# Optimization experiments

Measured on AMD Instinct MI355X. Metric: run time of the kernel, lower is better.

The kernel has to match this reference:

```python
import jax, jax.numpy as jnp
import numpy as np

BS, SEQ, VOCAB, EMS, NHID, ML = 32, 512, 5000, 256, 512, 16
TEMP = 0.9
GAMMA = 0.0  # self.gamma is a fixed zero Variable in the original


def setup_inputs() -> dict:
    key = jax.random.key(0)
    ks = jax.random.split(key, 10)
    nm = SEQ // ML
    inputs = jax.random.randint(ks[0], (BS, SEQ), 0, VOCAB, dtype=jnp.int32)
    measure_steps = jax.random.randint(ks[1], (ML, BS, nm), 0, VOCAB, dtype=jnp.int32)
    measure_weights = jax.random.normal(ks[2], (BS, nm, nm), dtype=jnp.float32)
    h0 = jnp.zeros((BS, NHID), jnp.float32)
    c0 = jnp.zeros((BS, NHID), jnp.float32)
    initrange = 0.1
    emb = jax.random.uniform(ks[3], (VOCAB, EMS), minval=-initrange, maxval=initrange)
    k = 1.0 / np.sqrt(NHID).astype(np.float32)
    W_ih = jax.random.uniform(ks[4], (4 * NHID, EMS), minval=-k, maxval=k)
    W_hh = jax.random.uniform(ks[5], (4 * NHID, NHID), minval=-k, maxval=k)
    b_ih = jax.random.uniform(ks[6], (4 * NHID,), minval=-k, maxval=k)
    b_hh = jax.random.uniform(ks[7], (4 * NHID,), minval=-k, maxval=k)
    W_dec = jax.random.uniform(ks[8], (VOCAB, NHID), minval=-initrange, maxval=initrange)
    b_dec = jnp.zeros((VOCAB,), jnp.float32)
    return dict(inputs=inputs, h0=h0, c0=c0, measure_weights=measure_weights,
                measure_steps=measure_steps, emb=emb, W_ih=W_ih, W_hh=W_hh,
                b_ih=b_ih, b_hh=b_hh, W_dec=W_dec, b_dec=b_dec, measure_length=ML)


def _forward(h0, c0, mw, emb, W_ih, W_hh, b_ih, b_hh, W_dec, b_dec,
             inputs, msteps, measure_length):
    bs, seq = inputs.shape
    nm = seq // measure_length
    # attention over previous measures: softmax over j < m (causal-masked)
    mask = (jnp.arange(nm)[None, :] < jnp.arange(nm)[:, None]).astype(mw.dtype)  # [m, j]
    logits = jnp.where(mask[None] > 0, mw / TEMP, -1e9)
    sm = jax.nn.softmax(logits, axis=-1) * mask[None]  # [bs, m, j]
    prev_embs = emb[msteps]  # [ML, bs, nm, E]
    # lookback embedding for (measure m, step s): sum_j sm[b,m,j] * emb[steps[s,b,j]]
    lb = jnp.einsum('bmj,sbje->msbe', sm, prev_embs)  # [nm, ML, bs, E]
    lb_seq = lb.reshape(seq, bs, -1)  # time-major: t = m*ML + s
    # per-step bmm decode against embedding table: [bs, seq, V]
    lookback = jnp.einsum('tbe,ve->btv', lb_seq, emb)
    # original zeros lookback for timesteps with int(i/num_measures)==0, i.e. i < nm
    tmask = (jnp.arange(seq) >= nm)[None, :, None]
    lookback = jnp.where(tmask, lookback, jnp.zeros((), lookback.dtype))

    x = emb[inputs]  # [bs, seq, E] (single channel -> concat is identity)

    def cell(carry, xt):
        h, c = carry
        g = xt @ W_ih.T + b_ih + h @ W_hh.T + b_hh
        i, f, gg, o = jnp.split(g, 4, axis=-1)
        c2 = jax.nn.sigmoid(f) * c + jax.nn.sigmoid(i) * jnp.tanh(gg)
        h2 = jax.nn.sigmoid(o) * jnp.tanh(c2)
        return (h2, c2), h2

    (hT, cT), hs = jax.lax.scan(cell, (h0, c0), jnp.swapaxes(x, 0, 1))
    out = jnp.swapaxes(hs, 0, 1)  # [bs, seq, nhid]
    decoded = out @ W_dec.T + b_dec  # [bs, seq, V]
    dec = (1.0 - GAMMA) * decoded + GAMMA * lookback
    return dec, hT, cT


def reference(inputs, h0, c0, measure_weights, measure_steps, emb,
              W_ih, W_hh, b_ih, b_hh, W_dec, b_dec, measure_length):
    return _forward(h0, c0, measure_weights, emb, W_ih, W_hh, b_ih, b_hh,
                    W_dec, b_dec, inputs, measure_steps, measure_length)
```

## Files before the change

kernel.cpp:

```cpp
#include <hip/hip_runtime.h>
#include <cstdint>
#include <cstddef>

#define BS     32
#define SEQ    512
#define VOCAB  5000
#define EMS    256
#define NHID   512
#define GH     2048
#define NWG    32
#define SLICE  16
#define VPAD   5120
#define NTILE  ((BS*SEQ/128) * (VPAD/128))

#define WS_BIAS  0
#define WS_WIH   (WS_BIAS + GH*4)
#define WS_WHH   (WS_WIH + GH*EMS*2)
#define WS_WDH   (WS_WHH + GH*NHID*2)
#define WS_WDL   (WS_WDH + VPAD*NHID*2)
#define WS_X     (WS_WDL + VPAD*NHID*2)
#define WS_HHI   (WS_X + SEQ*BS*EMS*2)
#define WS_HLO   (WS_HHI + BS*SEQ*NHID*2)
#define WS_TAG   (WS_HLO + BS*SEQ*NHID*2)
#define WS_END   (WS_TAG + 2*8192*8)

typedef float f32x4 __attribute__((ext_vector_type(4)));
typedef __bf16 bf16x8 __attribute__((ext_vector_type(8)));

static __device__ __forceinline__ uint16_t f2bf(float x) {
  uint32_t u = __builtin_bit_cast(uint32_t, x);
  u += 0x7FFFu + ((u >> 16) & 1u);
  return (uint16_t)(u >> 16);
}
static __device__ __forceinline__ float bf2f(uint16_t b) {
  return __builtin_bit_cast(float, (uint32_t)b << 16);
}
static __device__ __forceinline__ float sigf(float x) { return 1.0f / (1.0f + __expf(-x)); }
static __device__ __forceinline__ float tanhf_fast(float x) {
  return 1.0f - 2.0f / (__expf(2.0f * x) + 1.0f);
}
static __device__ __forceinline__ f32x4 mfma16(uint4 a, uint4 b, f32x4 c) {
  return __builtin_amdgcn_mfma_f32_16x16x32_bf16(
      __builtin_bit_cast(bf16x8, a), __builtin_bit_cast(bf16x8, b), c, 0, 0, 0);
}
static __device__ __forceinline__ void glds16(const void* g, void* l) {
  __builtin_amdgcn_global_load_lds((__attribute__((address_space(1))) void*)g,
                                   (__attribute__((address_space(3))) void*)l,
                                   16, 0, 0);
}

__global__ __launch_bounds__(256) void prep_kernel(
    const int* __restrict__ inputs, const float* __restrict__ h0,
    const float* __restrict__ emb, const float* __restrict__ Wih,
    const float* __restrict__ Whh, const float* __restrict__ bih,
    const float* __restrict__ bhh, const float* __restrict__ Wd,
    char* __restrict__ ws) {
  int gid = blockIdx.x * 256 + threadIdx.x;
  int gsz = gridDim.x * 256;
  uint16_t* wX  = (uint16_t*)(ws + WS_X);
  uint16_t* wIH = (uint16_t*)(ws + WS_WIH);
  uint16_t* wHH = (uint16_t*)(ws + WS_WHH);
  uint16_t* wDH = (uint16_t*)(ws + WS_WDH);
  uint16_t* wDL = (uint16_t*)(ws + WS_WDL);
  float*    bias = (float*)(ws + WS_BIAS);
  unsigned long long* Tg = (unsigned long long*)(ws + WS_TAG);
  for (int i = gid; i < SEQ*BS*EMS; i += gsz) {
    int e = i & (EMS-1), b = (i >> 8) & (BS-1), t = i >> 13;
    wX[i] = f2bf(emb[(size_t)inputs[b*SEQ + t] * EMS + e]);
  }
  for (int i = gid; i < GH*EMS; i += gsz)  wIH[i] = f2bf(Wih[i]);
  for (int i = gid; i < GH*NHID; i += gsz) wHH[i] = f2bf(Whh[i]);
  for (int i = gid; i < VPAD*NHID; i += gsz) {
    int row = i >> 9;
    uint16_t hi = 0, lo = 0;
    if (row < VOCAB) {
      float x = Wd[i];
      hi = f2bf(x);
      lo = f2bf(x - bf2f(hi));
    }
    wDH[i] = hi; wDL[i] = lo;
  }
  for (int i = gid; i < GH; i += gsz) bias[i] = bih[i] + bhh[i];
  for (int u = gid; u < 8192; u += gsz) {
    int b = u >> 8, p = u & 255;
    uint32_t pay = (uint32_t)f2bf(h0[b*NHID + 2*p]) |
                   ((uint32_t)f2bf(h0[b*NHID + 2*p + 1]) << 16);
    Tg[u] = (unsigned long long)pay;
    Tg[8192 + u] = 0xFFFFFFFF00000000ull;
  }
}

template <int KSTEPS, int NPASS>
__global__ __launch_bounds__(256) void gemm_kernel(
    const uint16_t* __restrict__ A0, const uint16_t* __restrict__ B0,
    const float* __restrict__ bias, float* __restrict__ out,
    int Nvalid, int ldout) {
  constexpr int K = KSTEPS * 32;
  constexpr int TOT = KSTEPS * NPASS;
  __shared__ __align__(16) char lds[4][8192];
  const int tid = threadIdx.x;
  const int lane = tid & 63, w = tid >> 6;
  const int m0 = blockIdx.y * 128, n0 = blockIdx.x * 128;
  const int wbase = (tid & ~63);

  auto stage = [&](int buf, int s) {
    const int kk = s % KSTEPS;
    char* dA = &lds[buf*2][0];
    char* dB = &lds[buf*2+1][0];
#pragma unroll
    for (int c = 0; c < 2; ++c) {
      int idx = c*256 + tid;
      int row = idx >> 2, col = (idx & 3) * 8;
      glds16(A0 + (size_t)(m0 + row) * K + kk*32 + col, dA + (c*256 + wbase)*16);
      glds16(B0 + (size_t)(n0 + row) * K + kk*32 + col, dB + (c*256 + wbase)*16);
    }
  };

  const f32x4 zero = {0.f, 0.f, 0.f, 0.f};
  f32x4 acc[4][4];
#pragma unroll
  for (int i = 0; i < 4; ++i)
#pragma unroll
    for (int j = 0; j < 4; ++j) acc[i][j] = zero;

  const int mq = (w >> 1) * 64, nq = (w & 1) * 64;
  stage(0, 0);
  for (int s = 0; s < TOT; ++s) {
    __syncthreads();
    if (s + 1 < TOT) stage((s + 1) & 1, s + 1);
    const char* cA = &lds[(s & 1)*2][0];
    const char* cB = &lds[(s & 1)*2+1][0];
    uint4 a[4], b[4];
#pragma unroll
    for (int i = 0; i < 4; ++i) {
      a[i] = *(const uint4*)(cA + (mq + i*16 + (lane & 15))*64 + (lane >> 4)*16);
      b[i] = *(const uint4*)(cB + (nq + i*16 + (lane & 15))*64 + (lane >> 4)*16);
    }
#pragma unroll
    for (int i = 0; i < 4; ++i)
#pragma unroll
      for (int j = 0; j < 4; ++j) acc[i][j] = mfma16(a[i], b[j], acc[i][j]);
  }
#pragma unroll
  for (int j = 0; j < 4; ++j) {
    int V = n0 + nq + j*16 + (lane & 15);
    if (V >= Nvalid) continue;
    float bv = bias[V];
#pragma unroll
    for (int i = 0; i < 4; ++i) {
      int Rb = m0 + mq + i*16 + (lane >> 4)*4;
#pragma unroll
      for (int r = 0; r < 4; ++r)
        out[(size_t)(Rb + r) * ldout + V] = acc[i][j][r] + bv;
    }
  }
}

__global__ __launch_bounds__(256, 1) void scan_kernel(
    const float* __restrict__ Gin, char* __restrict__ ws,
    const float* __restrict__ c0, float* __restrict__ outT) {
  __shared__ __align__(16) char sW[64*1024];
  __shared__ __align__(16) char sH[32*1024];
  __shared__ float sG[4*BS*SLICE];
  const uint16_t* wHH = (const uint16_t*)(ws + WS_WHH);
  unsigned long long* Tg = (unsigned long long*)(ws + WS_TAG);
  uint16_t* Hhi  = (uint16_t*)(ws + WS_HHI);
  uint16_t* Hlo  = (uint16_t*)(ws + WS_HLO);
  const int tid = threadIdx.x, wg = blockIdx.x;
  const int lane = tid & 63, w = tid >> 6;
  const int mw = w >> 1, nw = w & 1;

  for (int c = tid; c < 4096; c += 256) {
    int row = c >> 6;
    int kb = (c & 63) * 16;
    int G = row >> 4, dl = row & 15;
    uint4 v = *(const uint4*)(wHH + (size_t)(G*NHID + wg*SLICE + dl) * NHID + kb/2);
    *(uint4*)(sW + row*1024 + (kb ^ ((row & 7) << 4))) = v;
  }
  const int bq = tid >> 3, dq = (tid & 7) * 2;
  float c_0 = c0[bq*NHID + wg*SLICE + dq];
  float c_1 = c0[bq*NHID + wg*SLICE + dq + 1];
  const int arow = mw*16 + (lane & 15);
  const int brow0 = (2*nw)*16 + (lane & 15);
  const int brow1 = brow0 + 16;
  const int kb0 = (lane >> 4) * 16;
  const int pidx = bq*256 + wg*8 + (tid & 7);

  float ga0[4], ga1[4], gb0[4], gb1[4];
  {
    const float* grow = Gin + wg*SLICE + (lane & 15);
#pragma unroll
    for (int r = 0; r < 4; ++r) {
      int b = mw*16 + (lane >> 4)*4 + r;
      ga0[r] = grow[(size_t)b*GH + (2*nw+0)*NHID];
      ga1[r] = grow[(size_t)b*GH + (2*nw+1)*NHID];
    }
  }
  __syncthreads();

  for (int t = 0; t < SEQ; ++t) {
    if (t + 1 < SEQ) {
      const float* grow = Gin + (size_t)(t+1)*(BS*GH) + wg*SLICE + (lane & 15);
#pragma unroll
      for (int r = 0; r < 4; ++r) {
        int b = mw*16 + (lane >> 4)*4 + r;
        gb0[r] = grow[(size_t)b*GH + (2*nw+0)*NHID];
        gb1[r] = grow[(size_t)b*GH + (2*nw+1)*NHID];
      }
    }

    {
      const char* tb = (const char*)(Tg + (size_t)(t & 1) * 8192) + tid * 16;
      const uint32_t tg = (uint32_t)t;
      uint4 q0, q1, q2, q3, q4, q5, q6, q7, q8, q9, q10, q11, q12, q13, q14, q15;
      uint32_t tries = 0;
      for (;;) {
#define PQ(QJ, OFF) asm volatile("global_load_dwordx4 %0, %1, off sc0 sc1" \
                                 : "=v"(QJ) : "v"(tb + (OFF)));
        PQ(q0, 0)      PQ(q1, 4096)   PQ(q2, 8192)   PQ(q3, 12288)
        PQ(q4, 16384)  PQ(q5, 20480)  PQ(q6, 24576)  PQ(q7, 28672)
        PQ(q8, 32768)  PQ(q9, 36864)  PQ(q10, 40960) PQ(q11, 45056)
        PQ(q12, 49152) PQ(q13, 53248) PQ(q14, 57344) PQ(q15, 61440)
#undef PQ
        asm volatile("s_waitcnt vmcnt(0)" ::: "memory");
        __builtin_amdgcn_sched_barrier(0);
        uint32_t bad =
            (q0.y^tg)|(q0.w^tg)|(q1.y^tg)|(q1.w^tg)|(q2.y^tg)|(q2.w^tg)|(q3.y^tg)|(q3.w^tg)|
            (q4.y^tg)|(q4.w^tg)|(q5.y^tg)|(q5.w^tg)|(q6.y^tg)|(q6.w^tg)|(q7.y^tg)|(q7.w^tg)|
            (q8.y^tg)|(q8.w^tg)|(q9.y^tg)|(q9.w^tg)|(q10.y^tg)|(q10.w^tg)|(q11.y^tg)|(q11.w^tg)|
            (q12.y^tg)|(q12.w^tg)|(q13.y^tg)|(q13.w^tg)|(q14.y^tg)|(q14.w^tg)|(q15.y^tg)|(q15.w^tg);
        if (bad == 0) break;
        if (++tries > (1u << 16)) break;
      }
      const int colb = (tid & 127) * 8;
      const int rh = tid >> 7;
#define STW(J, QJ) { int b = 2*(J) + rh; uint2 wv; wv.x = QJ.x; wv.y = QJ.z; \
      *(uint2*)(sH + b*1024 + (colb ^ ((b & 7) << 4))) = wv; }
      STW(0, q0)   STW(1, q1)   STW(2, q2)   STW(3, q3)
      STW(4, q4)   STW(5, q5)   STW(6, q6)   STW(7, q7)
      STW(8, q8)   STW(9, q9)   STW(10, q10) STW(11, q11)
      STW(12, q12) STW(13, q13) STW(14, q14) STW(15, q15)
#undef STW
    }
    __syncthreads();

    f32x4 acc0, acc1;
#pragma unroll
    for (int r = 0; r < 4; ++r) { acc0[r] = ga0[r]; acc1[r] = ga1[r]; }
#pragma unroll
    for (int kt = 0; kt < 16; ++kt) {
      int kb = kt*64 + kb0;
      uint4 av = *(const uint4*)(sH + arow*1024 + (kb ^ ((arow & 7) << 4)));
      uint4 b0 = *(const uint4*)(sW + brow0*1024 + (kb ^ ((brow0 & 7) << 4)));
      uint4 b1 = *(const uint4*)(sW + brow1*1024 + (kb ^ ((brow1 & 7) << 4)));
      acc0 = mfma16(av, b0, acc0);
      acc1 = mfma16(av, b1, acc1);
    }
#pragma unroll
    for (int r = 0; r < 4; ++r) {
      int b = mw*16 + (lane >> 4)*4 + r;
      sG[((2*nw+0)*BS + b)*SLICE + (lane & 15)] = acc0[r];
      sG[((2*nw+1)*BS + b)*SLICE + (lane & 15)] = acc1[r];
    }
#pragma unroll
    for (int r = 0; r < 4; ++r) { ga0[r] = gb0[r]; ga1[r] = gb1[r]; }
    __syncthreads();

    float gi0 = sG[(0*BS + bq)*SLICE + dq], gi1 = sG[(0*BS + bq)*SLICE + dq + 1];
    float gf0 = sG[(1*BS + bq)*SLICE + dq], gf1 = sG[(1*BS + bq)*SLICE + dq + 1];
    float gg0 = sG[(2*BS + bq)*SLICE + dq], gg1 = sG[(2*BS + bq)*SLICE + dq + 1];
    float go0 = sG[(3*BS + bq)*SLICE + dq], go1 = sG[(3*BS + bq)*SLICE + dq + 1];
    c_0 = sigf(gf0)*c_0 + sigf(gi0)*tanhf_fast(gg0);
    c_1 = sigf(gf1)*c_1 + sigf(gi1)*tanhf_fast(gg1);
    float h_0 = sigf(go0)*tanhf_fast(c_0);
    float h_1 = sigf(go1)*tanhf_fast(c_1);

    uint16_t hh0 = f2bf(h_0), hh1 = f2bf(h_1);
    uint32_t hp = (uint32_t)hh0 | ((uint32_t)hh1 << 16);
    __hip_atomic_store(Tg + (size_t)((t + 1) & 1) * 8192 + pidx,
                       ((unsigned long long)(uint32_t)(t + 1) << 32) | (unsigned long long)hp,
                       __ATOMIC_RELAXED, __HIP_MEMORY_SCOPE_AGENT);
    size_t hoff = ((size_t)bq*SEQ + t)*NHID + wg*SLICE + dq;
    *(uint32_t*)(Hhi + hoff) = hp;
    uint32_t lp = (uint32_t)f2bf(h_0 - bf2f(hh0)) | ((uint32_t)f2bf(h_1 - bf2f(hh1)) << 16);
    *(uint32_t*)(Hlo + hoff) = lp;
    if (t == SEQ-1) {
      outT[bq*NHID + wg*SLICE + dq]     = h_0;
      outT[bq*NHID + wg*SLICE + dq + 1] = h_1;
      outT[BS*NHID + bq*NHID + wg*SLICE + dq]     = c_0;
      outT[BS*NHID + bq*NHID + wg*SLICE + dq + 1] = c_1;
    }
  }
}

__global__ __launch_bounds__(256) void decode_kernel(
    const char* __restrict__ ws, const float* __restrict__ bdec,
    float* __restrict__ out) {
  __shared__ __align__(16) char lds[2][32768];
  const uint16_t* Hhi = (const uint16_t*)(ws + WS_HHI);
  const uint16_t* Hlo = (const uint16_t*)(ws + WS_HLO);
  const uint16_t* WDH = (const uint16_t*)(ws + WS_WDH);
  const uint16_t* WDL = (const uint16_t*)(ws + WS_WDL);
  const int tid = threadIdx.x;
  const int lane = tid & 63, w = tid >> 6;
  const int wbase = (tid & ~63);
  const int mq = (w >> 1) * 64, nq = (w & 1) * 64;
  const int bid = (int)blockIdx.x;
  const int swz = (bid & 7) * (NTILE / 8) + (bid >> 3);
  const int mt = swz / 40, nt = swz % 40;
  const int m0 = mt * 128, n0 = nt * 128;

  auto stage = [&](int buf, int kk) {
    char* base = &lds[buf][0];
#pragma unroll
    for (int c2 = 0; c2 < 2; ++c2) {
      int idx = c2*256 + tid;
      int row = idx >> 2, col = (idx & 3) * 8;
      int ldst = (c2*256 + wbase) * 16;
      glds16(Hhi + (size_t)(m0 + row) * NHID + kk*32 + col, base + ldst);
      glds16(Hlo + (size_t)(m0 + row) * NHID + kk*32 + col, base + 8192 + ldst);
      glds16(WDH + (size_t)(n0 + row) * NHID + kk*32 + col, base + 16384 + ldst);
      glds16(WDL + (size_t)(n0 + row) * NHID + kk*32 + col, base + 24576 + ldst);
    }
  };

  const f32x4 zero = {0.f, 0.f, 0.f, 0.f};
  f32x4 acc[4][4];
#pragma unroll
  for (int i = 0; i < 4; ++i)
#pragma unroll
    for (int j = 0; j < 4; ++j) acc[i][j] = zero;

  stage(0, 0);
  for (int s = 0; s < 16; ++s) {
    __syncthreads();
    if (s + 1 < 16) stage((s + 1) & 1, s + 1);
    const char* cb = &lds[s & 1][0];
    uint4 ahi[4], alo[4], bhi[4], blo[4];
#pragma unroll
    for (int i = 0; i < 4; ++i) {
      int aoff = (mq + i*16 + (lane & 15))*64 + (lane >> 4)*16;
      int boff = (nq + i*16 + (lane & 15))*64 + (lane >> 4)*16;
      ahi[i] = *(const uint4*)(cb + aoff);
      alo[i] = *(const uint4*)(cb + 8192 + aoff);
      bhi[i] = *(const uint4*)(cb + 16384 + boff);
      blo[i] = *(const uint4*)(cb + 24576 + boff);
    }
#pragma unroll
    for (int i = 0; i < 4; ++i)
#pragma unroll
      for (int j = 0; j < 4; ++j) {
        acc[i][j] = mfma16(ahi[i], bhi[j], acc[i][j]);
        acc[i][j] = mfma16(ahi[i], blo[j], acc[i][j]);
        acc[i][j] = mfma16(alo[i], bhi[j], acc[i][j]);
      }
  }
#pragma unroll
  for (int j = 0; j < 4; ++j) {
    int V = n0 + nq + j*16 + (lane & 15);
    if (V >= VOCAB) continue;
    float bv = bdec[V];
#pragma unroll
    for (int i = 0; i < 4; ++i) {
      int Rb = m0 + mq + i*16 + (lane >> 4)*4;
#pragma unroll
      for (int r = 0; r < 4; ++r)
        out[(size_t)(Rb + r) * VOCAB + V] = acc[i][j][r] + bv;
    }
  }
}

extern "C" void kernel_launch(void* const* d_in, const int* in_sizes, int n_in,
                              void* d_out, int out_size, void* d_ws, size_t ws_size,
                              hipStream_t stream) {
  (void)in_sizes; (void)n_in; (void)out_size; (void)ws_size;
  const int*   inputs = (const int*)  d_in[0];
  const float* h0     = (const float*)d_in[1];
  const float* c0     = (const float*)d_in[2];
  const float* emb    = (const float*)d_in[5];
  const float* Wih    = (const float*)d_in[6];
  const float* Whh    = (const float*)d_in[7];
  const float* bih    = (const float*)d_in[8];
  const float* bhh    = (const float*)d_in[9];
  const float* Wdec   = (const float*)d_in[10];
  const float* bdec   = (const float*)d_in[11];
  char* ws   = (char*)d_ws;
  float* out = (float*)d_out;
  float* Gin  = out;
  float* outT = out + (size_t)BS*SEQ*VOCAB;

  prep_kernel<<<512, 256, 0, stream>>>(inputs, h0, emb, Wih, Whh, bih, bhh, Wdec, ws);
  gemm_kernel<8,1><<<dim3(GH/128, (BS*SEQ)/128), 256, 0, stream>>>(
      (const uint16_t*)(ws + WS_X), (const uint16_t*)(ws + WS_WIH),
      (const float*)(ws + WS_BIAS), Gin, GH, GH);
  scan_kernel<<<NWG, 256, 0, stream>>>(Gin, ws, c0, outT);
  decode_kernel<<<NTILE, 256, 0, stream>>>(ws, bdec, out);
}
```

Measured before the change: 2.050 ms.

## Re-lay h exchange buffer dim-major and re-poll only stale chunks

Changes the layout of the tagged cross-workgroup hidden-state exchange buffer from batch-major to hidden-pair-major, so each workgroup's published slice is contiguous and the LDS scatter pattern changes. The spin-wait loop now issues one initial load round, then reloads only the chunks whose tags are stale, with a wave-wide any() exit test. This is meant to cut redundant global traffic and latency in the per-timestep grid synchronisation of the LSTM recurrence. The LDS stores become 32-bit instead of 64-bit, which may add bank conflicts, and the retry limit is raised.

```diff
diff --git a/kernel.cpp b/kernel.cpp
--- a/kernel.cpp
+++ b/kernel.cpp
@@ -82,9 +82,9 @@
   }
   for (int i = gid; i < GH; i += gsz) bias[i] = bih[i] + bhh[i];
   for (int u = gid; u < 8192; u += gsz) {
-    int b = u >> 8, p = u & 255;
-    uint32_t pay = (uint32_t)f2bf(h0[b*NHID + 2*p]) |
-                   ((uint32_t)f2bf(h0[b*NHID + 2*p + 1]) << 16);
+    int dpair = u >> 5, b = u & 31;
+    uint32_t pay = (uint32_t)f2bf(h0[b*NHID + 2*dpair]) |
+                   ((uint32_t)f2bf(h0[b*NHID + 2*dpair + 1]) << 16);
     Tg[u] = (unsigned long long)pay;
     Tg[8192 + u] = 0xFFFFFFFF00000000ull;
   }
@@ -184,7 +184,7 @@
   const int brow0 = (2*nw)*16 + (lane & 15);
   const int brow1 = brow0 + 16;
   const int kb0 = (lane >> 4) * 16;
-  const int pidx = bq*256 + wg*8 + (tid & 7);
+  const int pidx = (wg*8 + (tid & 7))*32 + bq;
 
   float ga0[4], ga1[4], gb0[4], gb1[4];
   {
@@ -213,33 +213,49 @@
       const char* tb = (const char*)(Tg + (size_t)(t & 1) * 8192) + tid * 16;
       const uint32_t tg = (uint32_t)t;
       uint4 q0, q1, q2, q3, q4, q5, q6, q7, q8, q9, q10, q11, q12, q13, q14, q15;
+#define PQ(QJ, KT) asm volatile("global_load_dwordx4 %0, %1, off sc0 sc1" \
+                                : "=v"(QJ) : "v"(tb + (KT)*4096));
+      PQ(q0, 0)   PQ(q1, 1)   PQ(q2, 2)   PQ(q3, 3)
+      PQ(q4, 4)   PQ(q5, 5)   PQ(q6, 6)   PQ(q7, 7)
+      PQ(q8, 8)   PQ(q9, 9)   PQ(q10, 10) PQ(q11, 11)
+      PQ(q12, 12) PQ(q13, 13) PQ(q14, 14) PQ(q15, 15)
+      asm volatile("s_waitcnt vmcnt(0)" ::: "memory");
+      __builtin_amdgcn_sched_barrier(0);
+      uint32_t m;
       uint32_t tries = 0;
       for (;;) {
-#define PQ(QJ, OFF) asm volatile("global_load_dwordx4 %0, %1, off sc0 sc1" \
-                                 : "=v"(QJ) : "v"(tb + (OFF)));
-        PQ(q0, 0)      PQ(q1, 4096)   PQ(q2, 8192)   PQ(q3, 12288)
-        PQ(q4, 16384)  PQ(q5, 20480)  PQ(q6, 24576)  PQ(q7, 28672)
-        PQ(q8, 32768)  PQ(q9, 36864)  PQ(q10, 40960) PQ(q11, 45056)
-        PQ(q12, 49152) PQ(q13, 53248) PQ(q14, 57344) PQ(q15, 61440)
-#undef PQ
+        m = 0;
+#define CHK(QJ, KT) m |= ((((QJ).y ^ tg) | ((QJ).w ^ tg)) != 0u ? 1u : 0u) << (KT);
+        CHK(q0, 0)   CHK(q1, 1)   CHK(q2, 2)   CHK(q3, 3)
+        CHK(q4, 4)   CHK(q5, 5)   CHK(q6, 6)   CHK(q7, 7)
+        CHK(q8, 8)   CHK(q9, 9)   CHK(q10, 10) CHK(q11, 11)
+        CHK(q12, 12) CHK(q13, 13) CHK(q14, 14) CHK(q15, 15)
+#undef CHK
+        if (!__any((int)(m != 0u))) break;
+        if (++tries > (1u << 18)) break;
+#define RQ(QJ, KT) if (m & (1u << (KT))) PQ(QJ, KT)
+        RQ(q0, 0)   RQ(q1, 1)   RQ(q2, 2)   RQ(q3, 3)
+        RQ(q4, 4)   RQ(q5, 5)   RQ(q6, 6)   RQ(q7, 7)
+        RQ(q8, 8)   RQ(q9, 9)   RQ(q10, 10) RQ(q11, 11)
+        RQ(q12, 12) RQ(q13, 13) RQ(q14, 14) RQ(q15, 15)
+#undef RQ
         asm volatile("s_waitcnt vmcnt(0)" ::: "memory");
         __builtin_amdgcn_sched_barrier(0);
-        uint32_t bad =
-            (q0.y^tg)|(q0.w^tg)|(q1.y^tg)|(q1.w^tg)|(q2.y^tg)|(q2.w^tg)|(q3.y^tg)|(q3.w^tg)|
-            (q4.y^tg)|(q4.w^tg)|(q5.y^tg)|(q5.w^tg)|(q6.y^tg)|(q6.w^tg)|(q7.y^tg)|(q7.w^tg)|
-            (q8.y^tg)|(q8.w^tg)|(q9.y^tg)|(q9.w^tg)|(q10.y^tg)|(q10.w^tg)|(q11.y^tg)|(q11.w^tg)|
-            (q12.y^tg)|(q12.w^tg)|(q13.y^tg)|(q13.w^tg)|(q14.y^tg)|(q14.w^tg)|(q15.y^tg)|(q15.w^tg);
-        if (bad == 0) break;
-        if (++tries > (1u << 16)) break;
       }
-      const int colb = (tid & 127) * 8;
-      const int rh = tid >> 7;
-#define STW(J, QJ) { int b = 2*(J) + rh; uint2 wv; wv.x = QJ.x; wv.y = QJ.z; \
-      *(uint2*)(sH + b*1024 + (colb ^ ((b & 7) << 4))) = wv; }
-      STW(0, q0)   STW(1, q1)   STW(2, q2)   STW(3, q3)
-      STW(4, q4)   STW(5, q5)   STW(6, q6)   STW(7, q7)
-      STW(8, q8)   STW(9, q9)   STW(10, q10) STW(11, q11)
-      STW(12, q12) STW(13, q13) STW(14, q14) STW(15, q15)
+#undef PQ
+      const int b0 = 2 * (tid & 15);
+      const int cbase = (tid >> 4) * 4;
+      char* r0 = sH + b0*1024;
+      char* r1 = sH + (b0+1)*1024;
+      const int sw0 = (b0 & 7) << 4;
+      const int sw1 = ((b0+1) & 7) << 4;
+#define STW(QJ, KT) { int cb = (KT)*64 + cbase; \
+      *(uint32_t*)(r0 + (cb ^ sw0)) = (QJ).x; \
+      *(uint32_t*)(r1 + (cb ^ sw1)) = (QJ).z; }
+      STW(q0, 0)   STW(q1, 1)   STW(q2, 2)   STW(q3, 3)
+      STW(q4, 4)   STW(q5, 5)   STW(q6, 6)   STW(q7, 7)
+      STW(q8, 8)   STW(q9, 9)   STW(q10, 10) STW(q11, 11)
+      STW(q12, 12) STW(q13, 13) STW(q14, 14) STW(q15, 15)
 #undef STW
     }
     __syncthreads();
@@ -251,10 +267,10 @@
     for (int kt = 0; kt < 16; ++kt) {
       int kb = kt*64 + kb0;
       uint4 av = *(const uint4*)(sH + arow*1024 + (kb ^ ((arow & 7) << 4)));
-      uint4 b0 = *(const uint4*)(sW + brow0*1024 + (kb ^ ((brow0 & 7) << 4)));
-      uint4 b1 = *(const uint4*)(sW + brow1*1024 + (kb ^ ((brow1 & 7) << 4)));
-      acc0 = mfma16(av, b0, acc0);
-      acc1 = mfma16(av, b1, acc1);
+      uint4 b0v = *(const uint4*)(sW + brow0*1024 + (kb ^ ((brow0 & 7) << 4)));
+      uint4 b1v = *(const uint4*)(sW + brow1*1024 + (kb ^ ((brow1 & 7) << 4)));
+      acc0 = mfma16(av, b0v, acc0);
+      acc1 = mfma16(av, b1v, acc1);
     }
 #pragma unroll
     for (int r = 0; r < 4; ++r) {
```

Measured after the change: 2.339 ms. +14.1%, slower.

## Restructure LSTM scan into 64 single-wave workgroups split by batch half

Applied to the files above, without the earlier changes.

The recurrent scan now runs 64 single-wavefront workgroups, each owning a 16-hidden slice for one half of the batch, instead of 32 four-wave workgroups. Each wave computes all four gates with MFMA and applies the cell update straight from registers, which removes the LDS gate exchange and both __syncthreads per step. The tag buffer layout is regrouped per batch half so each wave polls only the 32 KB it needs, with a wave-wide any() check. The cost is twice as many workgroups polling and writing flags, plus shuffles to pack the bf16 pairs; each wave also loads the full 64 KB weight slice.

```diff
diff --git a/kernel.cpp b/kernel.cpp
--- a/kernel.cpp
+++ b/kernel.cpp
@@ -8,7 +8,6 @@
 #define EMS    256
 #define NHID   512
 #define GH     2048
-#define NWG    32
 #define SLICE  16
 #define VPAD   5120
 #define NTILE  ((BS*SEQ/128) * (VPAD/128))
@@ -82,9 +81,11 @@
   }
   for (int i = gid; i < GH; i += gsz) bias[i] = bih[i] + bhh[i];
   for (int u = gid; u < 8192; u += gsz) {
-    int b = u >> 8, p = u & 255;
-    uint32_t pay = (uint32_t)f2bf(h0[b*NHID + 2*p]) |
-                   ((uint32_t)f2bf(h0[b*NHID + 2*p + 1]) << 16);
+    int mm = u >> 12, n = u & 4095;
+    int D = n >> 4, bp = n & 15;
+    int b = mm*16 + bp;
+    uint32_t pay = (uint32_t)f2bf(h0[b*NHID + 2*D]) |
+                   ((uint32_t)f2bf(h0[b*NHID + 2*D + 1]) << 16);
     Tg[u] = (unsigned long long)pay;
     Tg[8192 + u] = 0xFFFFFFFF00000000ull;
   }
@@ -156,139 +157,140 @@
   }
 }
 
-__global__ __launch_bounds__(256, 1) void scan_kernel(
+__global__ __launch_bounds__(64, 1) void scan_kernel(
     const float* __restrict__ Gin, char* __restrict__ ws,
     const float* __restrict__ c0, float* __restrict__ outT) {
   __shared__ __align__(16) char sW[64*1024];
-  __shared__ __align__(16) char sH[32*1024];
-  __shared__ float sG[4*BS*SLICE];
+  __shared__ __align__(16) char sH[16*1024];
   const uint16_t* wHH = (const uint16_t*)(ws + WS_WHH);
   unsigned long long* Tg = (unsigned long long*)(ws + WS_TAG);
-  uint16_t* Hhi  = (uint16_t*)(ws + WS_HHI);
-  uint16_t* Hlo  = (uint16_t*)(ws + WS_HLO);
-  const int tid = threadIdx.x, wg = blockIdx.x;
-  const int lane = tid & 63, w = tid >> 6;
-  const int mw = w >> 1, nw = w & 1;
-
-  for (int c = tid; c < 4096; c += 256) {
+  uint16_t* Hhi = (uint16_t*)(ws + WS_HHI);
+  uint16_t* Hlo = (uint16_t*)(ws + WS_HLO);
+  const int lane = threadIdx.x;
+  const int s = (int)blockIdx.x & 31, m = (int)blockIdx.x >> 5;
+  for (int c = lane; c < 4096; c += 64) {
     int row = c >> 6;
     int kb = (c & 63) * 16;
-    int G = row >> 4, dl = row & 15;
-    uint4 v = *(const uint4*)(wHH + (size_t)(G*NHID + wg*SLICE + dl) * NHID + kb/2);
+    int g = row >> 4, dl = row & 15;
+    uint4 v = *(const uint4*)(wHH + (size_t)(g*NHID + s*SLICE + dl) * NHID + kb/2);
     *(uint4*)(sW + row*1024 + (kb ^ ((row & 7) << 4))) = v;
   }
-  const int bq = tid >> 3, dq = (tid & 7) * 2;
-  float c_0 = c0[bq*NHID + wg*SLICE + dq];
-  float c_1 = c0[bq*NHID + wg*SLICE + dq + 1];
-  const int arow = mw*16 + (lane & 15);
-  const int brow0 = (2*nw)*16 + (lane & 15);
-  const int brow1 = brow0 + 16;
-  const int kb0 = (lane >> 4) * 16;
-  const int pidx = bq*256 + wg*8 + (tid & 7);
-
-  float ga0[4], ga1[4], gb0[4], gb1[4];
-  {
-    const float* grow = Gin + wg*SLICE + (lane & 15);
-#pragma unroll
-    for (int r = 0; r < 4; ++r) {
-      int b = mw*16 + (lane >> 4)*4 + r;
-      ga0[r] = grow[(size_t)b*GH + (2*nw+0)*NHID];
-      ga1[r] = grow[(size_t)b*GH + (2*nw+1)*NHID];
-    }
-  }
-  __syncthreads();
+  const int il = lane & 15, kq = lane >> 4;
+  const int d = s*16 + il;
+  const int bbase = m*16 + kq*4;
+  float cst[4];
+#pragma unroll
+  for (int r = 0; r < 4; ++r) cst[r] = c0[(bbase + r)*NHID + d];
+  float ga[16], gb[16];
+#pragma unroll
+  for (int g = 0; g < 4; ++g)
+#pragma unroll
+    for (int r = 0; r < 4; ++r)
+      ga[g*4+r] = Gin[(size_t)(bbase + r)*GH + g*NHID + d];
+  const int b0r = (2*lane) & 15, b1r = b0r + 1;
+  char* sr0 = sH + b0r*1024;
+  char* sr1 = sH + b1r*1024;
+  const int sw0 = (b0r & 7) << 4, sw1 = (b1r & 7) << 4;
 
   for (int t = 0; t < SEQ; ++t) {
     if (t + 1 < SEQ) {
-      const float* grow = Gin + (size_t)(t+1)*(BS*GH) + wg*SLICE + (lane & 15);
-#pragma unroll
-      for (int r = 0; r < 4; ++r) {
-        int b = mw*16 + (lane >> 4)*4 + r;
-        gb0[r] = grow[(size_t)b*GH + (2*nw+0)*NHID];
-        gb1[r] = grow[(size_t)b*GH + (2*nw+1)*NHID];
-      }
-    }
-
+      const float* gr = Gin + (size_t)(t+1)*(BS*GH) + d;
+#pragma unroll
+      for (int g = 0; g < 4; ++g)
+#pragma unroll
+        for (int r = 0; r < 4; ++r)
+          gb[g*4+r] = gr[(size_t)(bbase + r)*GH + g*NHID];
+    }
     {
-      const char* tb = (const char*)(Tg + (size_t)(t & 1) * 8192) + tid * 16;
+      const char* tb = (const char*)(Tg + (size_t)(t & 1)*8192 + (size_t)m*4096) + lane*16;
       const uint32_t tg = (uint32_t)t;
-      uint4 q0, q1, q2, q3, q4, q5, q6, q7, q8, q9, q10, q11, q12, q13, q14, q15;
+      uint4 q0,q1,q2,q3,q4,q5,q6,q7,q8,q9,q10,q11,q12,q13,q14,q15;
+      uint4 q16,q17,q18,q19,q20,q21,q22,q23,q24,q25,q26,q27,q28,q29,q30,q31;
       uint32_t tries = 0;
       for (;;) {
-#define PQ(QJ, OFF) asm volatile("global_load_dwordx4 %0, %1, off sc0 sc1" \
-                                 : "=v"(QJ) : "v"(tb + (OFF)));
-        PQ(q0, 0)      PQ(q1, 4096)   PQ(q2, 8192)   PQ(q3, 12288)
-        PQ(q4, 16384)  PQ(q5, 20480)  PQ(q6, 24576)  PQ(q7, 28672)
-        PQ(q8, 32768)  PQ(q9, 36864)  PQ(q10, 40960) PQ(q11, 45056)
-        PQ(q12, 49152) PQ(q13, 53248) PQ(q14, 57344) PQ(q15, 61440)
+#define PQ(QJ, J) asm volatile("global_load_dwordx4 %0, %1, off sc0 sc1" \
+                               : "=v"(QJ) : "v"(tb + (J)*1024));
+        PQ(q0,0) PQ(q1,1) PQ(q2,2) PQ(q3,3) PQ(q4,4) PQ(q5,5) PQ(q6,6) PQ(q7,7)
+        PQ(q8,8) PQ(q9,9) PQ(q10,10) PQ(q11,11) PQ(q12,12) PQ(q13,13) PQ(q14,14) PQ(q15,15)
+        PQ(q16,16) PQ(q17,17) PQ(q18,18) PQ(q19,19) PQ(q20,20) PQ(q21,21) PQ(q22,22) PQ(q23,23)
+        PQ(q24,24) PQ(q25,25) PQ(q26,26) PQ(q27,27) PQ(q28,28) PQ(q29,29) PQ(q30,30) PQ(q31,31)
 #undef PQ
         asm volatile("s_waitcnt vmcnt(0)" ::: "memory");
         __builtin_amdgcn_sched_barrier(0);
         uint32_t bad =
-            (q0.y^tg)|(q0.w^tg)|(q1.y^tg)|(q1.w^tg)|(q2.y^tg)|(q2.w^tg)|(q3.y^tg)|(q3.w^tg)|
-            (q4.y^tg)|(q4.w^tg)|(q5.y^tg)|(q5.w^tg)|(q6.y^tg)|(q6.w^tg)|(q7.y^tg)|(q7.w^tg)|
-            (q8.y^tg)|(q8.w^tg)|(q9.y^tg)|(q9.w^tg)|(q10.y^tg)|(q10.w^tg)|(q11.y^tg)|(q11.w^tg)|
-            (q12.y^tg)|(q12.w^tg)|(q13.y^tg)|(q13.w^tg)|(q14.y^tg)|(q14.w^tg)|(q15.y^tg)|(q15.w^tg);
-        if (bad == 0) break;
-        if (++tries > (1u << 16)) break;
+          (q0.y^tg)|(q0.w^tg)|(q1.y^tg)|(q1.w^tg)|(q2.y^tg)|(q2.w^tg)|(q3.y^tg)|(q3.w^tg)|
+          (q4.y^tg)|(q4.w^tg)|(q5.y^tg)|(q5.w^tg)|(q6.y^tg)|(q6.w^tg)|(q7.y^tg)|(q7.w^tg)|
+          (q8.y^tg)|(q8.w^tg)|(q9.y^tg)|(q9.w^tg)|(q10.y^tg)|(q10.w^tg)|(q11.y^tg)|(q11.w^tg)|
+          (q12.y^tg)|(q12.w^tg)|(q13.y^tg)|(q13.w^tg)|(q14.y^tg)|(q14.w^tg)|(q15.y^tg)|(q15.w^tg)|
+          (q16.y^tg)|(q16.w^tg)|(q17.y^tg)|(q17.w^tg)|(q18.y^tg)|(q18.w^tg)|(q19.y^tg)|(q19.w^tg)|
+          (q20.y^tg)|(q20.w^tg)|(q21.y^tg)|(q21.w^tg)|(q22.y^tg)|(q22.w^tg)|(q23.y^tg)|(q23.w^tg)|
+          (q24.y^tg)|(q24.w^tg)|(q25.y^tg)|(q25.w^tg)|(q26.y^tg)|(q26.w^tg)|(q27.y^tg)|(q27.w^tg)|
+          (q28.y^tg)|(q28.w^tg)|(q29.y^tg)|(q29.w^tg)|(q30.y^tg)|(q30.w^tg)|(q31.y^tg)|(q31.w^tg);
+        if (!__any((int)(bad != 0u))) break;
+        if (++tries > (1u << 14)) break;
       }
-      const int colb = (tid & 127) * 8;
-      const int rh = tid >> 7;
-#define STW(J, QJ) { int b = 2*(J) + rh; uint2 wv; wv.x = QJ.x; wv.y = QJ.z; \
-      *(uint2*)(sH + b*1024 + (colb ^ ((b & 7) << 4))) = wv; }
-      STW(0, q0)   STW(1, q1)   STW(2, q2)   STW(3, q3)
-      STW(4, q4)   STW(5, q5)   STW(6, q6)   STW(7, q7)
-      STW(8, q8)   STW(9, q9)   STW(10, q10) STW(11, q11)
-      STW(12, q12) STW(13, q13) STW(14, q14) STW(15, q15)
+#define STW(QJ, J) { int cb = ((J)*8 + (lane >> 3)) * 4; \
+      *(uint32_t*)(sr0 + (cb ^ sw0)) = (QJ).x; \
+      *(uint32_t*)(sr1 + (cb ^ sw1)) = (QJ).z; }
+      STW(q0,0) STW(q1,1) STW(q2,2) STW(q3,3) STW(q4,4) STW(q5,5) STW(q6,6) STW(q7,7)
+      STW(q8,8) STW(q9,9) STW(q10,10) STW(q11,11) STW(q12,12) STW(q13,13) STW(q14,14) STW(q15,15)
+      STW(q16,16) STW(q17,17) STW(q18,18) STW(q19,19) STW(q20,20) STW(q21,21) STW(q22,22) STW(q23,23)
+      STW(q24,24) STW(q25,25) STW(q26,26) STW(q27,27) STW(q28,28) STW(q29,29) STW(q30,30) STW(q31,31)
 #undef STW
     }
-    __syncthreads();
-
-    f32x4 acc0, acc1;
-#pragma unroll
-    for (int r = 0; r < 4; ++r) { acc0[r] = ga0[r]; acc1[r] = ga1[r]; }
+    f32x4 a0, a1, a2, a3;
+#pragma unroll
+    for (int r = 0; r < 4; ++r) {
+      a0[r] = ga[0*4+r]; a1[r] = ga[1*4+r]; a2[r] = ga[2*4+r]; a3[r] = ga[3*4+r];
+    }
 #pragma unroll
     for (int kt = 0; kt < 16; ++kt) {
-      int kb = kt*64 + kb0;
-      uint4 av = *(const uint4*)(sH + arow*1024 + (kb ^ ((arow & 7) << 4)));
-      uint4 b0 = *(const uint4*)(sW + brow0*1024 + (kb ^ ((brow0 & 7) << 4)));
-      uint4 b1 = *(const uint4*)(sW + brow1*1024 + (kb ^ ((brow1 & 7) << 4)));
-      acc0 = mfma16(av, b0, acc0);
-      acc1 = mfma16(av, b1, acc1);
-    }
+      int kb = (kt*64 + kq*16) ^ ((il & 7) << 4);
+      uint4 av  = *(const uint4*)(sH + il*1024 + kb);
+      uint4 bv0 = *(const uint4*)(sW + (0*16 + il)*1024 + kb);
+      uint4 bv1 = *(const uint4*)(sW + (1*16 + il)*1024 + kb);
+      uint4 bv2 = *(const uint4*)(sW + (2*16 + il)*1024 + kb);
+      uint4 bv3 = *(const uint4*)(sW + (3*16 + il)*1024 + kb);
+      a0 = mfma16(av, bv0, a0);
+      a1 = mfma16(av, bv1, a1);
+      a2 = mfma16(av, bv2, a2);
+      a3 = mfma16(av, bv3, a3);
+    }
+#pragma unroll
+    for (int k = 0; k < 16; ++k) ga[k] = gb[k];
+
+    float hr[4];
 #pragma unroll
     for (int r = 0; r < 4; ++r) {
-      int b = mw*16 + (lane >> 4)*4 + r;
-      sG[((2*nw+0)*BS + b)*SLICE + (lane & 15)] = acc0[r];
-      sG[((2*nw+1)*BS + b)*SLICE + (lane & 15)] = acc1[r];
-    }
-#pragma unroll
-    for (int r = 0; r < 4; ++r) { ga0[r] = gb0[r]; ga1[r] = gb1[r]; }
-    __syncthreads();
-
-    float gi0 = sG[(0*BS + bq)*SLICE + dq], gi1 = sG[(0*BS + bq)*SLICE + dq + 1];
-    float gf0 = sG[(1*BS + bq)*SLICE + dq], gf1 = sG[(1*BS + bq)*SLICE + dq + 1];
-    float gg0 = sG[(2*BS + bq)*SLICE + dq], gg1 = sG[(2*BS + bq)*SLICE + dq + 1];
-    float go0 = sG[(3*BS + bq)*SLICE + dq], go1 = sG[(3*BS + bq)*SLICE + dq + 1];
-    c_0 = sigf(gf0)*c_0 + sigf(gi0)*tanhf_fast(gg0);
-    c_1 = sigf(gf1)*c_1 + sigf(gi1)*tanhf_fast(gg1);
-    float h_0 = sigf(go0)*tanhf_fast(c_0);
-    float h_1 = sigf(go1)*tanhf_fast(c_1);
-
-    uint16_t hh0 = f2bf(h_0), hh1 = f2bf(h_1);
-    uint32_t hp = (uint32_t)hh0 | ((uint32_t)hh1 << 16);
-    __hip_atomic_store(Tg + (size_t)((t + 1) & 1) * 8192 + pidx,
-                       ((unsigned long long)(uint32_t)(t + 1) << 32) | (unsigned long long)hp,
-                       __ATOMIC_RELAXED, __HIP_MEMORY_SCOPE_AGENT);
-    size_t hoff = ((size_t)bq*SEQ + t)*NHID + wg*SLICE + dq;
-    *(uint32_t*)(Hhi + hoff) = hp;
-    uint32_t lp = (uint32_t)f2bf(h_0 - bf2f(hh0)) | ((uint32_t)f2bf(h_1 - bf2f(hh1)) << 16);
-    *(uint32_t*)(Hlo + hoff) = lp;
+      float cv = sigf(a1[r])*cst[r] + sigf(a0[r])*tanhf_fast(a2[r]);
+      hr[r] = sigf(a3[r])*tanhf_fast(cv);
+      cst[r] = cv;
+    }
+#pragma unroll
+    for (int r = 0; r < 4; ++r) {
+      uint16_t hh = f2bf(hr[r]);
+      float lo = hr[r] - bf2f(hh);
+      float hn = __shfl_xor(hr[r], 1);
+      float ln = __shfl_xor(lo, 1);
+      if ((lane & 1) == 0) {
+        uint32_t pay = (uint32_t)hh | ((uint32_t)f2bf(hn) << 16);
+        uint32_t lop = (uint32_t)f2bf(lo) | ((uint32_t)f2bf(ln) << 16);
+        int bp = kq*4 + r;
+        int n = (s*8 + (il >> 1))*16 + bp;
+        __hip_atomic_store(Tg + (size_t)((t + 1) & 1)*8192 + (size_t)m*4096 + n,
+            ((unsigned long long)(uint32_t)(t + 1) << 32) | (unsigned long long)pay,
+            __ATOMIC_RELAXED, __HIP_MEMORY_SCOPE_AGENT);
+        size_t hoff = ((size_t)(m*16 + bp)*SEQ + t)*NHID + d;
+        *(uint32_t*)(Hhi + hoff) = pay;
+        *(uint32_t*)(Hlo + hoff) = lop;
+      }
+    }
     if (t == SEQ-1) {
-      outT[bq*NHID + wg*SLICE + dq]     = h_0;
-      outT[bq*NHID + wg*SLICE + dq + 1] = h_1;
-      outT[BS*NHID + bq*NHID + wg*SLICE + dq]     = c_0;
-      outT[BS*NHID + bq*NHID + wg*SLICE + dq + 1] = c_1;
+#pragma unroll
+      for (int r = 0; r < 4; ++r) {
+        outT[(bbase + r)*NHID + d] = hr[r];
+        outT[BS*NHID + (bbase + r)*NHID + d] = cst[r];
+      }
     }
   }
 }
@@ -393,6 +395,6 @@
   gemm_kernel<8,1><<<dim3(GH/128, (BS*SEQ)/128), 256, 0, stream>>>(
       (const uint16_t*)(ws + WS_X), (const uint16_t*)(ws + WS_WIH),
       (const float*)(ws + WS_BIAS), Gin, GH, GH);
-  scan_kernel<<<NWG, 256, 0, stream>>>(Gin, ws, c0, outT);
+  scan_kernel<<<64, 64, 0, stream>>>(Gin, ws, c0, outT);
   decode_kernel<<<NTILE, 256, 0, stream>>>(ws, bdec, out);
 }
```

Result: slower. 2.873 ms (+40.1%).

## Replace tagged h-payload polling with per-workgroup step flags and plain h buffer

Applied to the files above, without the earlier changes.

The recurrent scan no longer publishes each hidden-state pair as a 64-bit word carrying a step tag. Each workgroup now writes bf16 h into a double-buffered plain buffer, runs a block barrier, and then bumps its own step flag. Consumers spin on the 32 flags (one lane per workgroup) and then do a single non-retrying load of half the previous data volume. This cuts the polled bytes per step, but each step now needs two serial global round trips (flag poll, then data load) plus an extra barrier. There is also no release fence between the h stores and the relaxed flag store, so visibility ordering is not guaranteed.

```diff
diff --git a/kernel.cpp b/kernel.cpp
--- a/kernel.cpp
+++ b/kernel.cpp
@@ -13,7 +13,8 @@
 #define VPAD   5120
 #define NTILE  ((BS*SEQ/128) * (VPAD/128))
 
-#define WS_BIAS  0
+#define WS_FLAGS 0
+#define WS_BIAS  2048
 #define WS_WIH   (WS_BIAS + GH*4)
 #define WS_WHH   (WS_WIH + GH*EMS*2)
 #define WS_WDH   (WS_WHH + GH*NHID*2)
@@ -21,8 +22,8 @@
 #define WS_X     (WS_WDL + VPAD*NHID*2)
 #define WS_HHI   (WS_X + SEQ*BS*EMS*2)
 #define WS_HLO   (WS_HHI + BS*SEQ*NHID*2)
-#define WS_TAG   (WS_HLO + BS*SEQ*NHID*2)
-#define WS_END   (WS_TAG + 2*8192*8)
+#define WS_HBUF  (WS_HLO + BS*SEQ*NHID*2)
+#define WS_END   (WS_HBUF + 2*BS*NHID*2)
 
 typedef float f32x4 __attribute__((ext_vector_type(4)));
 typedef __bf16 bf16x8 __attribute__((ext_vector_type(8)));
@@ -47,6 +48,9 @@
   __builtin_amdgcn_global_load_lds((__attribute__((address_space(1))) void*)g,
                                    (__attribute__((address_space(3))) void*)l,
                                    16, 0, 0);
+}
+static __device__ __forceinline__ void coh_store_u32(uint32_t* p, uint32_t v) {
+  __hip_atomic_store(p, v, __ATOMIC_RELAXED, __HIP_MEMORY_SCOPE_AGENT);
 }
 
 __global__ __launch_bounds__(256) void prep_kernel(
@@ -63,7 +67,8 @@
   uint16_t* wDH = (uint16_t*)(ws + WS_WDH);
   uint16_t* wDL = (uint16_t*)(ws + WS_WDL);
   float*    bias = (float*)(ws + WS_BIAS);
-  unsigned long long* Tg = (unsigned long long*)(ws + WS_TAG);
+  uint16_t* hb  = (uint16_t*)(ws + WS_HBUF);
+  if (gid < 512) ((uint32_t*)(ws + WS_FLAGS))[gid] = 0u;
   for (int i = gid; i < SEQ*BS*EMS; i += gsz) {
     int e = i & (EMS-1), b = (i >> 8) & (BS-1), t = i >> 13;
     wX[i] = f2bf(emb[(size_t)inputs[b*SEQ + t] * EMS + e]);
@@ -81,13 +86,7 @@
     wDH[i] = hi; wDL[i] = lo;
   }
   for (int i = gid; i < GH; i += gsz) bias[i] = bih[i] + bhh[i];
-  for (int u = gid; u < 8192; u += gsz) {
-    int b = u >> 8, p = u & 255;
-    uint32_t pay = (uint32_t)f2bf(h0[b*NHID + 2*p]) |
-                   ((uint32_t)f2bf(h0[b*NHID + 2*p + 1]) << 16);
-    Tg[u] = (unsigned long long)pay;
-    Tg[8192 + u] = 0xFFFFFFFF00000000ull;
-  }
+  for (int i = gid; i < BS*NHID; i += gsz) hb[i] = f2bf(h0[i]);
 }
 
 template <int KSTEPS, int NPASS>
@@ -163,9 +162,10 @@
   __shared__ __align__(16) char sH[32*1024];
   __shared__ float sG[4*BS*SLICE];
   const uint16_t* wHH = (const uint16_t*)(ws + WS_WHH);
-  unsigned long long* Tg = (unsigned long long*)(ws + WS_TAG);
+  uint16_t* hbuf = (uint16_t*)(ws + WS_HBUF);
   uint16_t* Hhi  = (uint16_t*)(ws + WS_HHI);
   uint16_t* Hlo  = (uint16_t*)(ws + WS_HLO);
+  uint32_t* flags = (uint32_t*)(ws + WS_FLAGS);
   const int tid = threadIdx.x, wg = blockIdx.x;
   const int lane = tid & 63, w = tid >> 6;
   const int mw = w >> 1, nw = w & 1;
@@ -184,7 +184,6 @@
   const int brow0 = (2*nw)*16 + (lane & 15);
   const int brow1 = brow0 + 16;
   const int kb0 = (lane >> 4) * 16;
-  const int pidx = bq*256 + wg*8 + (tid & 7);
 
   float ga0[4], ga1[4], gb0[4], gb1[4];
   {
@@ -199,6 +198,17 @@
   __syncthreads();
 
   for (int t = 0; t < SEQ; ++t) {
+    if (t > 0) {
+      const uint32_t tgt = (uint32_t)t;
+      const uint32_t* fp = flags + (lane & 31) * 16;
+      uint32_t ptries = 0;
+      for (;;) {
+        uint32_t v = __hip_atomic_load(fp, __ATOMIC_RELAXED, __HIP_MEMORY_SCOPE_AGENT);
+        if (__all((int)(v >= tgt))) break;
+        if (++ptries > (1u << 20)) break;
+      }
+    }
+
     if (t + 1 < SEQ) {
       const float* grow = Gin + (size_t)(t+1)*(BS*GH) + wg*SLICE + (lane & 15);
 #pragma unroll
@@ -210,36 +220,24 @@
     }
 
     {
-      const char* tb = (const char*)(Tg + (size_t)(t & 1) * 8192) + tid * 16;
-      const uint32_t tg = (uint32_t)t;
-      uint4 q0, q1, q2, q3, q4, q5, q6, q7, q8, q9, q10, q11, q12, q13, q14, q15;
-      uint32_t tries = 0;
-      for (;;) {
-#define PQ(QJ, OFF) asm volatile("global_load_dwordx4 %0, %1, off sc0 sc1" \
-                                 : "=v"(QJ) : "v"(tb + (OFF)));
-        PQ(q0, 0)      PQ(q1, 4096)   PQ(q2, 8192)   PQ(q3, 12288)
-        PQ(q4, 16384)  PQ(q5, 20480)  PQ(q6, 24576)  PQ(q7, 28672)
-        PQ(q8, 32768)  PQ(q9, 36864)  PQ(q10, 40960) PQ(q11, 45056)
-        PQ(q12, 49152) PQ(q13, 53248) PQ(q14, 57344) PQ(q15, 61440)
-#undef PQ
-        asm volatile("s_waitcnt vmcnt(0)" ::: "memory");
-        __builtin_amdgcn_sched_barrier(0);
-        uint32_t bad =
-            (q0.y^tg)|(q0.w^tg)|(q1.y^tg)|(q1.w^tg)|(q2.y^tg)|(q2.w^tg)|(q3.y^tg)|(q3.w^tg)|
-            (q4.y^tg)|(q4.w^tg)|(q5.y^tg)|(q5.w^tg)|(q6.y^tg)|(q6.w^tg)|(q7.y^tg)|(q7.w^tg)|
-            (q8.y^tg)|(q8.w^tg)|(q9.y^tg)|(q9.w^tg)|(q10.y^tg)|(q10.w^tg)|(q11.y^tg)|(q11.w^tg)|
-            (q12.y^tg)|(q12.w^tg)|(q13.y^tg)|(q13.w^tg)|(q14.y^tg)|(q14.w^tg)|(q15.y^tg)|(q15.w^tg);
-        if (bad == 0) break;
-        if (++tries > (1u << 16)) break;
-      }
-      const int colb = (tid & 127) * 8;
-      const int rh = tid >> 7;
-#define STW(J, QJ) { int b = 2*(J) + rh; uint2 wv; wv.x = QJ.x; wv.y = QJ.z; \
-      *(uint2*)(sH + b*1024 + (colb ^ ((b & 7) << 4))) = wv; }
-      STW(0, q0)   STW(1, q1)   STW(2, q2)   STW(3, q3)
-      STW(4, q4)   STW(5, q5)   STW(6, q6)   STW(7, q7)
-      STW(8, q8)   STW(9, q9)   STW(10, q10) STW(11, q11)
-      STW(12, q12) STW(13, q13) STW(14, q14) STW(15, q15)
+      const char* hsrc = (const char*)(hbuf + (t & 1) * (BS*NHID));
+      const char* pb = hsrc + tid * 16;
+      uint4 v0, v1, v2, v3, v4, v5, v6, v7;
+      asm volatile("global_load_dwordx4 %0, %1, off sc0 sc1" : "=v"(v0) : "v"(pb));
+      asm volatile("global_load_dwordx4 %0, %1, off sc0 sc1" : "=v"(v1) : "v"(pb + 4096));
+      asm volatile("global_load_dwordx4 %0, %1, off sc0 sc1" : "=v"(v2) : "v"(pb + 8192));
+      asm volatile("global_load_dwordx4 %0, %1, off sc0 sc1" : "=v"(v3) : "v"(pb + 12288));
+      asm volatile("global_load_dwordx4 %0, %1, off sc0 sc1" : "=v"(v4) : "v"(pb + 16384));
+      asm volatile("global_load_dwordx4 %0, %1, off sc0 sc1" : "=v"(v5) : "v"(pb + 20480));
+      asm volatile("global_load_dwordx4 %0, %1, off sc0 sc1" : "=v"(v6) : "v"(pb + 24576));
+      asm volatile("global_load_dwordx4 %0, %1, off sc0 sc1" : "=v"(v7) : "v"(pb + 28672));
+      asm volatile("s_waitcnt vmcnt(0)" ::: "memory");
+      __builtin_amdgcn_sched_barrier(0);
+      const int kb = (tid & 63) * 16;
+      const int ww = tid >> 6;
+#define STW(J, VJ) *(uint4*)(sH + ((J)*4 + ww)*1024 + (kb ^ ((((J)&1)*4 + ww) << 4))) = VJ;
+      STW(0, v0) STW(1, v1) STW(2, v2) STW(3, v3)
+      STW(4, v4) STW(5, v5) STW(6, v6) STW(7, v7)
 #undef STW
     }
     __syncthreads();
@@ -277,9 +275,14 @@
 
     uint16_t hh0 = f2bf(h_0), hh1 = f2bf(h_1);
     uint32_t hp = (uint32_t)hh0 | ((uint32_t)hh1 << 16);
-    __hip_atomic_store(Tg + (size_t)((t + 1) & 1) * 8192 + pidx,
-                       ((unsigned long long)(uint32_t)(t + 1) << 32) | (unsigned long long)hp,
-                       __ATOMIC_RELAXED, __HIP_MEMORY_SCOPE_AGENT);
+    coh_store_u32((uint32_t*)(hbuf + ((t+1) & 1)*(BS*NHID)) +
+                      ((bq*NHID + wg*SLICE + dq) >> 1), hp);
+
+    __syncthreads();
+    if (tid == 0)
+      __hip_atomic_store(flags + wg * 16, (uint32_t)(t + 1),
+                         __ATOMIC_RELAXED, __HIP_MEMORY_SCOPE_AGENT);
+
     size_t hoff = ((size_t)bq*SEQ + t)*NHID + wg*SLICE + dq;
     *(uint32_t*)(Hhi + hoff) = hp;
     uint32_t lp = (uint32_t)f2bf(h_0 - bf2f(hh0)) | ((uint32_t)f2bf(h_1 - bf2f(hh1)) << 16);
```

After: 1.847 ms (median of 2 runs). -9.9%, faster.
